# Kernel tuning notes

Hardware: AMD Instinct MI355X
Metric: run time of the kernel (lower is better)

Reference implementation:

```python
import jax, jax.numpy as jnp
import numpy as np

DIM = 256
NUM_HEADS = 8
REGIONS = [4, 4, 8, 8, 16, 16, 32, 32]  # per-head local window sizes
B, H_IMG, W_IMG = 8, 64, 64


def setup_inputs() -> dict:
    key = jax.random.key(0)
    ks = jax.random.split(key, 6)
    C = DIM
    s = 0.02
    return {
        'x': jax.random.normal(ks[0], (B, H_IMG * W_IMG, C), jnp.float32),
        'Wq': jax.random.normal(ks[1], (C, C), jnp.float32) * s,
        'Wkv': jax.random.normal(ks[2], (C, 2 * C), jnp.float32) * s,
        'Wlkv': jax.random.normal(ks[3], (C, 2 * C), jnp.float32) * s,
        'Wproj': jax.random.normal(ks[4], (C, C), jnp.float32) * s,
        'bproj': jnp.zeros((C,), jnp.float32),
        'H': H_IMG,
        'W': W_IMG,
    }


def _attn(q, k, v, scale):
    # softmax(q k^T * scale) v, batched over leading dims
    a = jax.nn.softmax(jnp.einsum('...qd,...kd->...qk', q, k) * scale, axis=-1)
    return jnp.einsum('...qk,...kd->...qd', a, v)


def reference(x, Wq, Wkv, Wlkv, Wproj, bproj, H, W):
    Bn, N, C = x.shape
    nh = NUM_HEADS
    Ch = C // nh
    scale = Ch ** -0.5
    M = max(REGIONS)

    q = (x @ Wq).reshape(Bn, N, nh, Ch).transpose(0, 2, 1, 3)            # [B,nh,N,Ch]
    kv = (x @ Wkv).reshape(Bn, N, 2, nh, Ch).transpose(2, 0, 3, 1, 4)    # [2,B,nh,N,Ch]
    k, v = kv[0], kv[1]

    head_outs, global_q = [], []
    for i, p in enumerate(REGIONS):
        def patch(a, p=p):  # [B,N,Ch] -> [B,NP,p*p,Ch]
            a = a.reshape(Bn, H // p, p, W // p, p, Ch)
            return a.transpose(0, 1, 3, 2, 4, 5).reshape(Bn, -1, p * p, Ch)
        qp, kp, vp = patch(q[:, i]), patch(k[:, i]), patch(v[:, i])
        # global query: mean over patches -> [B,p,p,Ch], bilinear upsample to [M,M]
        qg = qp.mean(axis=1).reshape(Bn, p, p, Ch)
        if M // p > 1:
            qg = jax.image.resize(qg, (Bn, M, M, Ch), method='bilinear')
        global_q.append(qg.reshape(Bn, M * M, Ch))
        out = _attn(qp, kp, vp, scale)                                    # [B,NP,p*p,Ch]
        head_outs.append(out.reshape(Bn, N, Ch))  # flatten in PATCH order (matches torch code)

    attn_fused = jnp.stack(head_outs, axis=1).transpose(0, 2, 1, 3).reshape(Bn, N, C)
    Q_g = jnp.stack(global_q, axis=1).transpose(0, 2, 1, 3).reshape(Bn, M * M, C)

    # blend: adaptive avg-pool attn_fused to [M,M] (exact pooling since M|H), cross-attend, upsample
    kh, kw = H // M, W // M
    pooled = attn_fused.reshape(Bn, M, kh, M, kw, C).mean(axis=(2, 4)).reshape(Bn, M * M, C)
    kv2 = (pooled @ Wlkv).reshape(Bn, M * M, 2, nh, Ch).transpose(2, 0, 3, 1, 4)
    k2, v2 = kv2[0], kv2[1]
    Qr = Q_g.reshape(Bn, M * M, nh, Ch).transpose(0, 2, 1, 3)             # [B,nh,M^2,Ch]
    gl = _attn(Qr, k2, v2, scale)                                          # [B,nh,M^2,Ch]
    gl = gl.transpose(0, 2, 1, 3).reshape(Bn, M, M, C)
    gl = jax.image.resize(gl, (Bn, H, W, C), method='bilinear').reshape(Bn, N, C)

    return (attn_fused + gl) @ Wproj + bproj
```

## Files before the change

### kernel.cpp

```cpp
#include <hip/hip_runtime.h>
#include <math.h>


typedef __attribute__((ext_vector_type(8))) short bf16x8;
typedef __attribute__((ext_vector_type(4))) float f32x4;

__device__ inline float bf2f(unsigned short u) {
  union { unsigned int i; float f; } v; v.i = ((unsigned int)u) << 16; return v.f;
}
__device__ inline unsigned short f2bf(float x) {
  union { float f; unsigned int i; } v; v.f = x;
  return (unsigned short)((v.i + 0x7FFFu + ((v.i >> 16) & 1u)) >> 16);
}

__global__ __launch_bounds__(256) void msa_xcast_r12(
    const float* __restrict__ x, unsigned short* __restrict__ xb)
{
  const size_t i = ((size_t)blockIdx.x * 256 + threadIdx.x) * 8;
  const float4 v0 = *reinterpret_cast<const float4*>(&x[i]);
  const float4 v1 = *reinterpret_cast<const float4*>(&x[i + 4]);
  bf16x8 o;
  o[0] = (short)f2bf(v0.x); o[1] = (short)f2bf(v0.y);
  o[2] = (short)f2bf(v0.z); o[3] = (short)f2bf(v0.w);
  o[4] = (short)f2bf(v1.x); o[5] = (short)f2bf(v1.y);
  o[6] = (short)f2bf(v1.z); o[7] = (short)f2bf(v1.w);
  *reinterpret_cast<bf16x8*>(&xb[i]) = o;
}

__global__ __launch_bounds__(256) void msa_wcast_r12(
    const float* __restrict__ Wq, const float* __restrict__ Wkv,
    const float* __restrict__ Wlkv, const float* __restrict__ Wproj,
    unsigned short* __restrict__ Wqkvt, unsigned short* __restrict__ Wlkvt,
    unsigned short* __restrict__ Wprjt)
{
  const int id = blockIdx.x * 256 + threadIdx.x;
  if (id < 196608) {
    const int r = id >> 8, k = id & 255;
    const float v = (r < 256) ? Wq[(size_t)k * 256 + r] : Wkv[(size_t)k * 512 + (r - 256)];
    Wqkvt[id] = f2bf(v);
  } else if (id < 327680) {
    const int j = id - 196608;
    const int n = j >> 8, k = j & 255;
    Wlkvt[j] = f2bf(Wlkv[(size_t)k * 512 + n]);
  } else if (id < 393216) {
    const int j = id - 327680;
    const int n = j >> 8, k = j & 255;
    Wprjt[j] = f2bf(Wproj[(size_t)k * 256 + n]);
  }
}

__global__ __launch_bounds__(256) void msa_gemm_mfma_r12(
    const unsigned short* __restrict__ Ab, const unsigned short* __restrict__ Wt,
    const float* __restrict__ bias, float* __restrict__ Cf,
    unsigned short* __restrict__ Cb, int K, int N)
{
  __shared__ __align__(16) unsigned short A_lds[128][40];
  __shared__ __align__(16) unsigned short B_lds[128][40];

  const int tid = threadIdx.x;
  const int wave = tid >> 6, lane = tid & 63;
  const int l15 = lane & 15, g = lane >> 4;
  const int bm = blockIdx.y * 128, bn = blockIdx.x * 128;
  const int wr = (wave >> 1) * 64, wc = (wave & 1) * 64;

  f32x4 acc[4][4] = {};

  for (int k0 = 0; k0 < K; k0 += 32) {
    __syncthreads();
#pragma unroll
    for (int s = 0; s < 2; ++s) {
      const int id = tid + s * 256;
      const int row = id >> 2, sg = (id & 3) << 3;
      *reinterpret_cast<bf16x8*>(&A_lds[row][sg]) =
          *reinterpret_cast<const bf16x8*>(&Ab[(size_t)(bm + row) * K + k0 + sg]);
      *reinterpret_cast<bf16x8*>(&B_lds[row][sg]) =
          *reinterpret_cast<const bf16x8*>(&Wt[(size_t)(bn + row) * K + k0 + sg]);
    }
    __syncthreads();

    bf16x8 a_frag[4], b_frag[4];
#pragma unroll
    for (int mi = 0; mi < 4; ++mi)
      a_frag[mi] = *reinterpret_cast<const bf16x8*>(&A_lds[wr + mi * 16 + l15][g << 3]);
#pragma unroll
    for (int ni = 0; ni < 4; ++ni)
      b_frag[ni] = *reinterpret_cast<const bf16x8*>(&B_lds[wc + ni * 16 + l15][g << 3]);
#pragma unroll
    for (int mi = 0; mi < 4; ++mi)
#pragma unroll
      for (int ni = 0; ni < 4; ++ni)
        acc[mi][ni] = __builtin_amdgcn_mfma_f32_16x16x32_bf16(
            a_frag[mi], b_frag[ni], acc[mi][ni], 0, 0, 0);
  }

#pragma unroll
  for (int mi = 0; mi < 4; ++mi)
#pragma unroll
    for (int ni = 0; ni < 4; ++ni) {
      const int col = bn + wc + ni * 16 + l15;
#pragma unroll
      for (int i = 0; i < 4; ++i) {
        const int row = bm + wr + mi * 16 + g * 4 + i;
        float v = acc[mi][ni][i];
        if (bias) v += bias[col];
        const size_t idx = (size_t)row * N + col;
        if (Cb) Cb[idx] = f2bf(v); else Cf[idx] = v;
      }
    }
}

__global__ __launch_bounds__(256) void msa_attn_mfma_r12(
    const unsigned short* __restrict__ qsrc, const unsigned short* __restrict__ kvsrc,
    float* __restrict__ outf, unsigned short* __restrict__ outb, int mode)
{
  __shared__ __align__(16) unsigned short K_lds[32][40];
  __shared__ __align__(16) unsigned short V_lds[32][40];
  __shared__ __align__(16) unsigned short P_lds[4][16][40];

  const int tid = threadIdx.x;
  const int wave = tid >> 6, lane = tid & 63;
  const int q16 = lane & 15, h = lane >> 4;
  const int b = blockIdx.y;

  int head, NTOK, P2, lp, pm1, base, qstr, kvstr, kofs, vofs;
  if (mode) {
    head = blockIdx.z; NTOK = 1024; P2 = 1024; lp = 0; pm1 = 0; base = 0;
    qstr = 256; kvstr = 512; kofs = 0; vofs = 256;
  } else {
    head = 2 + blockIdx.z;
    lp = (head < 4) ? 3 : (head < 6) ? 4 : 5;
    const int p = 1 << lp; pm1 = p - 1;
    NTOK = 4096; P2 = p * p;
    const int patch = (blockIdx.x * 64) >> (2 * lp);
    const int nbp = 64 >> lp;
    const int hb = patch / nbp, wb = patch - (patch / nbp) * nbp;
    base = ((hb << lp)) * 64 + (wb << lp);
    qstr = 768; kvstr = 768; kofs = 256; vofs = 512;
  }
  const int nq = blockIdx.x * 64 + wave * 16 + q16;
  int n;
  if (mode) n = nq;
  else { const int t = nq & (P2 - 1); n = base + ((t >> lp) << 6) + (t & pm1); }

  const bf16x8 qfrag = *reinterpret_cast<const bf16x8*>(
      qsrc + ((size_t)b * NTOK + n) * qstr + head * 32 + 8 * h);

  const float scale = 0.17677669529663687f;
  float m = -3.0e38f, l = 0.f;
  f32x4 o0 = {0.f, 0.f, 0.f, 0.f}, o1 = {0.f, 0.f, 0.f, 0.f};
  const f32x4 zc = {0.f, 0.f, 0.f, 0.f};

  const int skey = (tid & 127) >> 2;
  const int sh = tid & 3;
  const bool isK = tid < 128;

  for (int kc = 0; kc < P2; kc += 32) {
    __syncthreads();
    {
      const int kk = kc + skey;
      const int nk = mode ? kk : base + ((kk >> lp) << 6) + (kk & pm1);
      const unsigned short* src = kvsrc + ((size_t)b * NTOK + nk) * kvstr + head * 32
                                + (isK ? kofs : vofs) + 8 * sh;
      const bf16x8 v = *reinterpret_cast<const bf16x8*>(src);
      if (isK) {
        *reinterpret_cast<bf16x8*>(&K_lds[skey][8 * sh]) = v;
      } else {
#pragma unroll
        for (int j = 0; j < 8; ++j)
          V_lds[8 * sh + j][skey] = (unsigned short)v[j];
      }
    }
    __syncthreads();

    const bf16x8 k0 = *reinterpret_cast<const bf16x8*>(&K_lds[q16][8 * h]);
    const bf16x8 k1 = *reinterpret_cast<const bf16x8*>(&K_lds[16 + q16][8 * h]);
    const f32x4 st0 = __builtin_amdgcn_mfma_f32_16x16x32_bf16(k0, qfrag, zc, 0, 0, 0);
    const f32x4 st1 = __builtin_amdgcn_mfma_f32_16x16x32_bf16(k1, qfrag, zc, 0, 0, 0);

    float s[8];
#pragma unroll
    for (int i = 0; i < 4; ++i) { s[i] = st0[i] * scale; s[4 + i] = st1[i] * scale; }
    float cmax = s[0];
#pragma unroll
    for (int i = 1; i < 8; ++i) cmax = fmaxf(cmax, s[i]);
    cmax = fmaxf(cmax, __shfl_xor(cmax, 16));
    cmax = fmaxf(cmax, __shfl_xor(cmax, 32));
    const float mnew = fmaxf(m, cmax);
    const float f = __expf(m - mnew);
    float ps = 0.f;
    unsigned short pb[8];
#pragma unroll
    for (int i = 0; i < 8; ++i) {
      const float pe = __expf(s[i] - mnew);
      ps += pe;
      pb[i] = f2bf(pe);
    }
    l = l * f + ps;
    o0 *= f; o1 *= f;
    m = mnew;

    *reinterpret_cast<uint2*>(&P_lds[wave][q16][4 * h]) =
        make_uint2((unsigned)pb[0] | ((unsigned)pb[1] << 16),
                   (unsigned)pb[2] | ((unsigned)pb[3] << 16));
    *reinterpret_cast<uint2*>(&P_lds[wave][q16][16 + 4 * h]) =
        make_uint2((unsigned)pb[4] | ((unsigned)pb[5] << 16),
                   (unsigned)pb[6] | ((unsigned)pb[7] << 16));

    const bf16x8 pf = *reinterpret_cast<const bf16x8*>(&P_lds[wave][q16][8 * h]);
    const bf16x8 v0 = *reinterpret_cast<const bf16x8*>(&V_lds[q16][8 * h]);
    const bf16x8 v1 = *reinterpret_cast<const bf16x8*>(&V_lds[16 + q16][8 * h]);
    o0 = __builtin_amdgcn_mfma_f32_16x16x32_bf16(v0, pf, o0, 0, 0, 0);
    o1 = __builtin_amdgcn_mfma_f32_16x16x32_bf16(v1, pf, o1, 0, 0, 0);
  }

  l = l + __shfl_xor(l, 16);
  l = l + __shfl_xor(l, 32);
  const float inv = 1.f / l;
  const size_t obase = ((size_t)b * NTOK + nq) * 256 + head * 32;
  if (mode) {
    float* dst = outf + obase;
    float4 w0, w1;
    w0.x = o0[0] * inv; w0.y = o0[1] * inv; w0.z = o0[2] * inv; w0.w = o0[3] * inv;
    w1.x = o1[0] * inv; w1.y = o1[1] * inv; w1.z = o1[2] * inv; w1.w = o1[3] * inv;
    *reinterpret_cast<float4*>(dst + 4 * h) = w0;
    *reinterpret_cast<float4*>(dst + 16 + 4 * h) = w1;
  } else {
    unsigned short* dst = outb + obase;
    uint2 w0, w1;
    w0.x = (unsigned)f2bf(o0[0] * inv) | ((unsigned)f2bf(o0[1] * inv) << 16);
    w0.y = (unsigned)f2bf(o0[2] * inv) | ((unsigned)f2bf(o0[3] * inv) << 16);
    w1.x = (unsigned)f2bf(o1[0] * inv) | ((unsigned)f2bf(o1[1] * inv) << 16);
    w1.y = (unsigned)f2bf(o1[2] * inv) | ((unsigned)f2bf(o1[3] * inv) << 16);
    *reinterpret_cast<uint2*>(dst + 4 * h) = w0;
    *reinterpret_cast<uint2*>(dst + 16 + 4 * h) = w1;
  }
}

__global__ __launch_bounds__(256) void msa_attn_p4_r12(
    const unsigned short* __restrict__ xqkv, unsigned short* __restrict__ out)
{
  const int head = blockIdx.z;
  const int b = blockIdx.y;
  const int nq = blockIdx.x * 256 + threadIdx.x;

  const int patch = nq >> 4;
  const int t = nq & 15;
  const int hb = patch >> 4, wb = patch & 15;
  const int n = (hb * 4 + (t >> 2)) * 64 + (wb * 4 + (t & 3));

  float qr[32];
  {
    const bf16x8* q8 = reinterpret_cast<const bf16x8*>(
        xqkv + ((size_t)b * 4096 + n) * 768 + head * 32);
#pragma unroll
    for (int i = 0; i < 4; ++i) {
      const bf16x8 v = q8[i];
#pragma unroll
      for (int j = 0; j < 8; ++j) qr[i * 8 + j] = bf2f((unsigned short)v[j]);
    }
  }
  const float scale = 0.17677669529663687f;
  float m = -3.0e38f, l = 0.f;
  float acc[32] = {};
  const int kbase = (hb * 4) * 64 + wb * 4;
  for (int kk = 0; kk < 16; ++kk) {
    const int nk = kbase + (kk >> 2) * 64 + (kk & 3);
    const unsigned short* rowp = xqkv + ((size_t)b * 4096 + nk) * 768 + head * 32;
    const bf16x8* k8p = reinterpret_cast<const bf16x8*>(rowp + 256);
    const bf16x8* v8p = reinterpret_cast<const bf16x8*>(rowp + 512);
    float s = 0.f;
#pragma unroll
    for (int i = 0; i < 4; ++i) {
      const bf16x8 k8 = k8p[i];
#pragma unroll
      for (int j = 0; j < 8; ++j) s = fmaf(qr[i * 8 + j], bf2f((unsigned short)k8[j]), s);
    }
    s *= scale;
    if (s <= m) {
      const float pe = __expf(s - m);
      l += pe;
#pragma unroll
      for (int i = 0; i < 4; ++i) {
        const bf16x8 v8 = v8p[i];
#pragma unroll
        for (int j = 0; j < 8; ++j)
          acc[i * 8 + j] = fmaf(pe, bf2f((unsigned short)v8[j]), acc[i * 8 + j]);
      }
    } else {
      const float f = __expf(m - s);
      l = fmaf(l, f, 1.f);
#pragma unroll
      for (int i = 0; i < 4; ++i) {
        const bf16x8 v8 = v8p[i];
#pragma unroll
        for (int j = 0; j < 8; ++j)
          acc[i * 8 + j] = fmaf(acc[i * 8 + j], f, bf2f((unsigned short)v8[j]));
      }
      m = s;
    }
  }
  const float inv = 1.f / l;
  unsigned short* dst = out + ((size_t)b * 4096 + nq) * 256 + head * 32;
#pragma unroll
  for (int c = 0; c < 32; ++c) dst[c] = f2bf(acc[c] * inv);
}

__global__ __launch_bounds__(256) void msa_qg_reduce_r12(
    const unsigned short* __restrict__ xqkv, float* __restrict__ qg_all)
{
  __shared__ float red[256];
  const int head = blockIdx.z;
  const int lp = (head < 2) ? 2 : (head < 4) ? 3 : (head < 6) ? 4 : 5;
  const int p = 1 << lp;
  const int P2 = p * p;
  const int nbp = 64 >> lp;
  const int npat = nbp * nbp;
  const int R = (lp <= 3) ? 8 : 1;
  const int total = P2 * 32 * R;
  const int gid = blockIdx.x * 256 + threadIdx.x;
  if (gid >= total) return;
  const int b = blockIdx.y;

  const int c = gid & 31;
  const int tr = gid >> 5;
  const int r = tr & (R - 1);
  const int t = tr >> ((R == 8) ? 3 : 0);
  const int hp = t >> lp, wp = t & (p - 1);

  const unsigned short* src = xqkv + (size_t)b * 4096 * 768 + head * 32 + c;
  float s = 0.f;
  for (int j = r; j < npat; j += R) {
    const int hb = j / nbp, wb = j - (j / nbp) * nbp;
    const int n = ((hb << lp) + hp) * 64 + (wb << lp) + wp;
    s += bf2f(src[(size_t)n * 768]);
  }

  if (R == 8) {
    red[threadIdx.x] = s;
    __syncthreads();
    if (r < 4) red[threadIdx.x] += red[threadIdx.x + 128];
    __syncthreads();
    if (r < 2) red[threadIdx.x] += red[threadIdx.x + 64];
    __syncthreads();
    if (r == 0) {
      s = red[threadIdx.x] + red[threadIdx.x + 32];
      qg_all[((size_t)b * 8 + head) * 32768 + (size_t)t * 32 + c] = s / (float)npat;
    }
  } else {
    qg_all[((size_t)b * 8 + head) * 32768 + (size_t)t * 32 + c] = s / (float)npat;
  }
}

__global__ __launch_bounds__(256) void msa_qg_upsample_r12(
    const float* __restrict__ qg_all, unsigned short* __restrict__ Qg)
{
  const int head = blockIdx.z;
  const int p = (head < 2) ? 4 : (head < 4) ? 8 : (head < 6) ? 16 : 32;
  const int e = blockIdx.x * 256 + threadIdx.x;
  const int b = blockIdx.y;
  const int mlin = e >> 5, c = e & 31;
  const int mi = mlin >> 5, mj = mlin & 31;
  const float* src = qg_all + ((size_t)b * 8 + head) * 32768;
  float v;
  if (p == 32) {
    v = src[(size_t)mlin * 32 + c];
  } else {
    const float s = (float)p / 32.0f;
    const float xf = (mj + 0.5f) * s - 0.5f;
    const float yf = (mi + 0.5f) * s - 0.5f;
    const float xfl = floorf(xf), yfl = floorf(yf);
    const float fx = xf - xfl, fy = yf - yfl;
    const int x0 = (int)xfl, y0 = (int)yfl;
    const int x0c = max(0, min(p - 1, x0)), x1c = max(0, min(p - 1, x0 + 1));
    const int y0c = max(0, min(p - 1, y0)), y1c = max(0, min(p - 1, y0 + 1));
    const float v00 = src[(size_t)(y0c * p + x0c) * 32 + c];
    const float v01 = src[(size_t)(y0c * p + x1c) * 32 + c];
    const float v10 = src[(size_t)(y1c * p + x0c) * 32 + c];
    const float v11 = src[(size_t)(y1c * p + x1c) * 32 + c];
    v = (1.f - fy) * ((1.f - fx) * v00 + fx * v01)
      + fy * ((1.f - fx) * v10 + fx * v11);
  }
  Qg[((size_t)b * 1024 + mlin) * 256 + head * 32 + c] = f2bf(v);
}

__global__ __launch_bounds__(256) void msa_pool_r12(
    const unsigned short* __restrict__ attn, unsigned short* __restrict__ pooled)
{
  const int c = threadIdx.x;
  const int mlin = blockIdx.x;
  const int b = blockIdx.y;
  const int mi = mlin >> 5, mj = mlin & 31;
  const size_t base = (size_t)b * 4096;
  const int r0 = mi * 2, q0 = mj * 2;
  float s = bf2f(attn[(base + (r0 * 64 + q0)) * 256 + c])
          + bf2f(attn[(base + (r0 * 64 + q0 + 1)) * 256 + c])
          + bf2f(attn[(base + ((r0 + 1) * 64 + q0)) * 256 + c])
          + bf2f(attn[(base + ((r0 + 1) * 64 + q0 + 1)) * 256 + c]);
  pooled[((size_t)b * 1024 + mlin) * 256 + c] = f2bf(s * 0.25f);
}

__global__ __launch_bounds__(256) void msa_blend_r12(
    const float* __restrict__ gl, unsigned short* __restrict__ attn)
{
  const int c = threadIdx.x;
  const int n = blockIdx.x;
  const int b = blockIdx.y;
  const int hh = n >> 6, w = n & 63;
  const float xf = (w + 0.5f) * 0.5f - 0.5f;
  const float yf = (hh + 0.5f) * 0.5f - 0.5f;
  const float xfl = floorf(xf), yfl = floorf(yf);
  const float fx = xf - xfl, fy = yf - yfl;
  const int x0 = (int)xfl, y0 = (int)yfl;
  const int x0c = max(0, min(31, x0)), x1c = max(0, min(31, x0 + 1));
  const int y0c = max(0, min(31, y0)), y1c = max(0, min(31, y0 + 1));
  const float* g = gl + (size_t)b * 1024 * 256;
  const float v00 = g[(size_t)(y0c * 32 + x0c) * 256 + c];
  const float v01 = g[(size_t)(y0c * 32 + x1c) * 256 + c];
  const float v10 = g[(size_t)(y1c * 32 + x0c) * 256 + c];
  const float v11 = g[(size_t)(y1c * 32 + x1c) * 256 + c];
  const float v = (1.f - fy) * ((1.f - fx) * v00 + fx * v01)
                + fy * ((1.f - fx) * v10 + fx * v11);
  const size_t idx = ((size_t)b * 4096 + n) * 256 + c;
  attn[idx] = f2bf(bf2f(attn[idx]) + v);
}

extern "C" void kernel_launch(void* const* d_in, const int* in_sizes, int n_in,
                              void* d_out, int out_size, void* d_ws, size_t ws_size,
                              hipStream_t stream)
{
  const float* x     = (const float*)d_in[0];
  const float* Wq    = (const float*)d_in[1];
  const float* Wkv   = (const float*)d_in[2];
  const float* Wlkv  = (const float*)d_in[3];
  const float* Wproj = (const float*)d_in[4];
  const float* bproj = (const float*)d_in[5];

  char* ws = (char*)d_ws;
  unsigned short* xqkv  = (unsigned short*)(ws + 0);
  unsigned short* attnb = (unsigned short*)(ws + 50331648ull);
  unsigned short* Qg    = (unsigned short*)(ws + 67108864ull);
  float* qg_all = (float*)(ws + 71303168ull);
  unsigned short* Wqkvt = (unsigned short*)(ws + 79691776ull);
  unsigned short* Wlkvt = (unsigned short*)(ws + 80084992ull);
  unsigned short* Wprjt = (unsigned short*)(ws + 80347136ull);
  float* gl     = (float*)(ws + 80478208ull);
  unsigned short* xb    = (unsigned short*)(ws + 88866816ull);
  unsigned short* pooled = (unsigned short*)(ws + 0);
  unsigned short* kv2    = (unsigned short*)(ws + 16777216ull);

  msa_xcast_r12<<<dim3(4096), 256, 0, stream>>>(x, xb);
  msa_wcast_r12<<<dim3(1536), 256, 0, stream>>>(Wq, Wkv, Wlkv, Wproj, Wqkvt, Wlkvt, Wprjt);

  msa_gemm_mfma_r12<<<dim3(6, 256), 256, 0, stream>>>(xb, Wqkvt, nullptr, nullptr, xqkv, 256, 768);

  msa_qg_reduce_r12<<<dim3(128, 8, 8), 256, 0, stream>>>(xqkv, qg_all);
  msa_qg_upsample_r12<<<dim3(128, 8, 8), 256, 0, stream>>>(qg_all, Qg);

  msa_attn_p4_r12<<<dim3(16, 8, 2), 256, 0, stream>>>(xqkv, attnb);
  msa_attn_mfma_r12<<<dim3(64, 8, 6), 256, 0, stream>>>(xqkv, xqkv, nullptr, attnb, 0);

  msa_pool_r12<<<dim3(1024, 8), 256, 0, stream>>>(attnb, pooled);
  msa_gemm_mfma_r12<<<dim3(4, 64), 256, 0, stream>>>(pooled, Wlkvt, nullptr, nullptr, kv2, 256, 512);

  msa_attn_mfma_r12<<<dim3(16, 8, 8), 256, 0, stream>>>(Qg, kv2, gl, nullptr, 1);

  msa_blend_r12<<<dim3(4096, 8), 256, 0, stream>>>(gl, attnb);
  msa_gemm_mfma_r12<<<dim3(2, 256), 256, 0, stream>>>(attnb, Wprjt, bproj, (float*)d_out, nullptr, 256, 256);

  (void)in_sizes; (void)n_in; (void)out_size; (void)ws_size;
}
```

Measured before the change: 235.2 us.

## Drop online-softmax max tracking and feed P directly from registers to MFMA

```diff
diff --git a/kernel.cpp b/kernel.cpp
--- a/kernel.cpp
+++ b/kernel.cpp
@@ -3,6 +3,7 @@
 
 
 typedef __attribute__((ext_vector_type(8))) short bf16x8;
+typedef __attribute__((ext_vector_type(4))) short bf16x4;
 typedef __attribute__((ext_vector_type(4))) float f32x4;
 
 __device__ inline float bf2f(unsigned short u) {
@@ -13,7 +14,7 @@
   return (unsigned short)((v.i + 0x7FFFu + ((v.i >> 16) & 1u)) >> 16);
 }
 
-__global__ __launch_bounds__(256) void msa_xcast_r12(
+__global__ __launch_bounds__(256) void msa_xcast_r13(
     const float* __restrict__ x, unsigned short* __restrict__ xb)
 {
   const size_t i = ((size_t)blockIdx.x * 256 + threadIdx.x) * 8;
@@ -27,7 +28,7 @@
   *reinterpret_cast<bf16x8*>(&xb[i]) = o;
 }
 
-__global__ __launch_bounds__(256) void msa_wcast_r12(
+__global__ __launch_bounds__(256) void msa_wcast_r13(
     const float* __restrict__ Wq, const float* __restrict__ Wkv,
     const float* __restrict__ Wlkv, const float* __restrict__ Wproj,
     unsigned short* __restrict__ Wqkvt, unsigned short* __restrict__ Wlkvt,
@@ -49,7 +50,7 @@
   }
 }
 
-__global__ __launch_bounds__(256) void msa_gemm_mfma_r12(
+__global__ __launch_bounds__(256) void msa_gemm_mfma_r13(
     const unsigned short* __restrict__ Ab, const unsigned short* __restrict__ Wt,
     const float* __restrict__ bias, float* __restrict__ Cf,
     unsigned short* __restrict__ Cb, int K, int N)
@@ -109,13 +110,12 @@
     }
 }
 
-__global__ __launch_bounds__(256) void msa_attn_mfma_r12(
+__global__ __launch_bounds__(256) void msa_attn_mfma_r13(
     const unsigned short* __restrict__ qsrc, const unsigned short* __restrict__ kvsrc,
     float* __restrict__ outf, unsigned short* __restrict__ outb, int mode)
 {
-  __shared__ __align__(16) unsigned short K_lds[32][40];
-  __shared__ __align__(16) unsigned short V_lds[32][40];
-  __shared__ __align__(16) unsigned short P_lds[4][16][40];
+  __shared__ __align__(16) unsigned short K_lds[64][40];
+  __shared__ __align__(16) unsigned short V_lds[32][68];
 
   const int tid = threadIdx.x;
   const int wave = tid >> 6, lane = tid & 63;
@@ -145,72 +145,60 @@
   const bf16x8 qfrag = *reinterpret_cast<const bf16x8*>(
       qsrc + ((size_t)b * NTOK + n) * qstr + head * 32 + 8 * h);
 
-  const float scale = 0.17677669529663687f;
-  float m = -3.0e38f, l = 0.f;
+  const float CEXP = 0.25503485947f;
+  float l = 0.f;
   f32x4 o0 = {0.f, 0.f, 0.f, 0.f}, o1 = {0.f, 0.f, 0.f, 0.f};
   const f32x4 zc = {0.f, 0.f, 0.f, 0.f};
 
-  const int skey = (tid & 127) >> 2;
+  const int skey = tid >> 2;
   const int sh = tid & 3;
-  const bool isK = tid < 128;
-
-  for (int kc = 0; kc < P2; kc += 32) {
+
+  for (int kc = 0; kc < P2; kc += 64) {
     __syncthreads();
     {
       const int kk = kc + skey;
       const int nk = mode ? kk : base + ((kk >> lp) << 6) + (kk & pm1);
-      const unsigned short* src = kvsrc + ((size_t)b * NTOK + nk) * kvstr + head * 32
-                                + (isK ? kofs : vofs) + 8 * sh;
-      const bf16x8 v = *reinterpret_cast<const bf16x8*>(src);
-      if (isK) {
-        *reinterpret_cast<bf16x8*>(&K_lds[skey][8 * sh]) = v;
-      } else {
-#pragma unroll
-        for (int j = 0; j < 8; ++j)
-          V_lds[8 * sh + j][skey] = (unsigned short)v[j];
+      const unsigned short* row = kvsrc + ((size_t)b * NTOK + nk) * kvstr + head * 32;
+      *reinterpret_cast<bf16x8*>(&K_lds[skey][8 * sh]) =
+          *reinterpret_cast<const bf16x8*>(row + kofs + 8 * sh);
+      const bf16x8 v = *reinterpret_cast<const bf16x8*>(row + vofs + 8 * sh);
+#pragma unroll
+      for (int j = 0; j < 8; ++j)
+        V_lds[8 * sh + j][skey] = (unsigned short)v[j];
+    }
+    __syncthreads();
+
+#pragma unroll
+    for (int sub = 0; sub < 2; ++sub) {
+      const int s32 = sub * 32;
+      const bf16x8 k0 = *reinterpret_cast<const bf16x8*>(&K_lds[s32 + q16][8 * h]);
+      const bf16x8 k1 = *reinterpret_cast<const bf16x8*>(&K_lds[s32 + 16 + q16][8 * h]);
+      const f32x4 st0 = __builtin_amdgcn_mfma_f32_16x16x32_bf16(k0, qfrag, zc, 0, 0, 0);
+      const f32x4 st1 = __builtin_amdgcn_mfma_f32_16x16x32_bf16(k1, qfrag, zc, 0, 0, 0);
+
+      bf16x8 pb;
+#pragma unroll
+      for (int i = 0; i < 4; ++i) {
+        const float p0 = exp2f(st0[i] * CEXP);
+        const float p1 = exp2f(st1[i] * CEXP);
+        l += p0 + p1;
+        pb[i] = (short)f2bf(p0);
+        pb[4 + i] = (short)f2bf(p1);
       }
-    }
-    __syncthreads();
-
-    const bf16x8 k0 = *reinterpret_cast<const bf16x8*>(&K_lds[q16][8 * h]);
-    const bf16x8 k1 = *reinterpret_cast<const bf16x8*>(&K_lds[16 + q16][8 * h]);
-    const f32x4 st0 = __builtin_amdgcn_mfma_f32_16x16x32_bf16(k0, qfrag, zc, 0, 0, 0);
-    const f32x4 st1 = __builtin_amdgcn_mfma_f32_16x16x32_bf16(k1, qfrag, zc, 0, 0, 0);
-
-    float s[8];
-#pragma unroll
-    for (int i = 0; i < 4; ++i) { s[i] = st0[i] * scale; s[4 + i] = st1[i] * scale; }
-    float cmax = s[0];
-#pragma unroll
-    for (int i = 1; i < 8; ++i) cmax = fmaxf(cmax, s[i]);
-    cmax = fmaxf(cmax, __shfl_xor(cmax, 16));
-    cmax = fmaxf(cmax, __shfl_xor(cmax, 32));
-    const float mnew = fmaxf(m, cmax);
-    const float f = __expf(m - mnew);
-    float ps = 0.f;
-    unsigned short pb[8];
-#pragma unroll
-    for (int i = 0; i < 8; ++i) {
-      const float pe = __expf(s[i] - mnew);
-      ps += pe;
-      pb[i] = f2bf(pe);
-    }
-    l = l * f + ps;
-    o0 *= f; o1 *= f;
-    m = mnew;
-
-    *reinterpret_cast<uint2*>(&P_lds[wave][q16][4 * h]) =
-        make_uint2((unsigned)pb[0] | ((unsigned)pb[1] << 16),
-                   (unsigned)pb[2] | ((unsigned)pb[3] << 16));
-    *reinterpret_cast<uint2*>(&P_lds[wave][q16][16 + 4 * h]) =
-        make_uint2((unsigned)pb[4] | ((unsigned)pb[5] << 16),
-                   (unsigned)pb[6] | ((unsigned)pb[7] << 16));
-
-    const bf16x8 pf = *reinterpret_cast<const bf16x8*>(&P_lds[wave][q16][8 * h]);
-    const bf16x8 v0 = *reinterpret_cast<const bf16x8*>(&V_lds[q16][8 * h]);
-    const bf16x8 v1 = *reinterpret_cast<const bf16x8*>(&V_lds[16 + q16][8 * h]);
-    o0 = __builtin_amdgcn_mfma_f32_16x16x32_bf16(v0, pf, o0, 0, 0, 0);
-    o1 = __builtin_amdgcn_mfma_f32_16x16x32_bf16(v1, pf, o1, 0, 0, 0);
+
+      const bf16x4 va0 = *reinterpret_cast<const bf16x4*>(&V_lds[q16][s32 + 4 * h]);
+      const bf16x4 vb0 = *reinterpret_cast<const bf16x4*>(&V_lds[q16][s32 + 16 + 4 * h]);
+      const bf16x4 va1 = *reinterpret_cast<const bf16x4*>(&V_lds[16 + q16][s32 + 4 * h]);
+      const bf16x4 vb1 = *reinterpret_cast<const bf16x4*>(&V_lds[16 + q16][s32 + 16 + 4 * h]);
+      bf16x8 v0, v1;
+#pragma unroll
+      for (int i = 0; i < 4; ++i) {
+        v0[i] = va0[i]; v0[4 + i] = vb0[i];
+        v1[i] = va1[i]; v1[4 + i] = vb1[i];
+      }
+      o0 = __builtin_amdgcn_mfma_f32_16x16x32_bf16(v0, pb, o0, 0, 0, 0);
+      o1 = __builtin_amdgcn_mfma_f32_16x16x32_bf16(v1, pb, o1, 0, 0, 0);
+    }
   }
 
   l = l + __shfl_xor(l, 16);
@@ -236,7 +224,7 @@
   }
 }
 
-__global__ __launch_bounds__(256) void msa_attn_p4_r12(
+__global__ __launch_bounds__(256) void msa_attn_p4_r13(
     const unsigned short* __restrict__ xqkv, unsigned short* __restrict__ out)
 {
   const int head = blockIdx.z;
@@ -259,8 +247,8 @@
       for (int j = 0; j < 8; ++j) qr[i * 8 + j] = bf2f((unsigned short)v[j]);
     }
   }
-  const float scale = 0.17677669529663687f;
-  float m = -3.0e38f, l = 0.f;
+  const float CEXP = 0.25503485947f;
+  float l = 0.f;
   float acc[32] = {};
   const int kbase = (hb * 4) * 64 + wb * 4;
   for (int kk = 0; kk < 16; ++kk) {
@@ -275,28 +263,14 @@
 #pragma unroll
       for (int j = 0; j < 8; ++j) s = fmaf(qr[i * 8 + j], bf2f((unsigned short)k8[j]), s);
     }
-    s *= scale;
-    if (s <= m) {
-      const float pe = __expf(s - m);
-      l += pe;
-#pragma unroll
-      for (int i = 0; i < 4; ++i) {
-        const bf16x8 v8 = v8p[i];
-#pragma unroll
-        for (int j = 0; j < 8; ++j)
-          acc[i * 8 + j] = fmaf(pe, bf2f((unsigned short)v8[j]), acc[i * 8 + j]);
-      }
-    } else {
-      const float f = __expf(m - s);
-      l = fmaf(l, f, 1.f);
-#pragma unroll
-      for (int i = 0; i < 4; ++i) {
-        const bf16x8 v8 = v8p[i];
-#pragma unroll
-        for (int j = 0; j < 8; ++j)
-          acc[i * 8 + j] = fmaf(acc[i * 8 + j], f, bf2f((unsigned short)v8[j]));
-      }
-      m = s;
+    const float p = exp2f(s * CEXP);
+    l += p;
+#pragma unroll
+    for (int i = 0; i < 4; ++i) {
+      const bf16x8 v8 = v8p[i];
+#pragma unroll
+      for (int j = 0; j < 8; ++j)
+        acc[i * 8 + j] = fmaf(p, bf2f((unsigned short)v8[j]), acc[i * 8 + j]);
     }
   }
   const float inv = 1.f / l;
@@ -305,7 +279,7 @@
   for (int c = 0; c < 32; ++c) dst[c] = f2bf(acc[c] * inv);
 }
 
-__global__ __launch_bounds__(256) void msa_qg_reduce_r12(
+__global__ __launch_bounds__(256) void msa_qg_reduce_r13(
     const unsigned short* __restrict__ xqkv, float* __restrict__ qg_all)
 {
   __shared__ float red[256];
@@ -351,7 +325,7 @@
   }
 }
 
-__global__ __launch_bounds__(256) void msa_qg_upsample_r12(
+__global__ __launch_bounds__(256) void msa_qg_upsample_r13(
     const float* __restrict__ qg_all, unsigned short* __restrict__ Qg)
 {
   const int head = blockIdx.z;
@@ -383,7 +357,7 @@
   Qg[((size_t)b * 1024 + mlin) * 256 + head * 32 + c] = f2bf(v);
 }
 
-__global__ __launch_bounds__(256) void msa_pool_r12(
+__global__ __launch_bounds__(256) void msa_pool_r13(
     const unsigned short* __restrict__ attn, unsigned short* __restrict__ pooled)
 {
   const int c = threadIdx.x;
@@ -399,7 +373,7 @@
   pooled[((size_t)b * 1024 + mlin) * 256 + c] = f2bf(s * 0.25f);
 }
 
-__global__ __launch_bounds__(256) void msa_blend_r12(
+__global__ __launch_bounds__(256) void msa_blend_r13(
     const float* __restrict__ gl, unsigned short* __restrict__ attn)
 {
   const int c = threadIdx.x;
@@ -448,24 +422,24 @@
   unsigned short* pooled = (unsigned short*)(ws + 0);
   unsigned short* kv2    = (unsigned short*)(ws + 16777216ull);
 
-  msa_xcast_r12<<<dim3(4096), 256, 0, stream>>>(x, xb);
-  msa_wcast_r12<<<dim3(1536), 256, 0, stream>>>(Wq, Wkv, Wlkv, Wproj, Wqkvt, Wlkvt, Wprjt);
-
-  msa_gemm_mfma_r12<<<dim3(6, 256), 256, 0, stream>>>(xb, Wqkvt, nullptr, nullptr, xqkv, 256, 768);
-
-  msa_qg_reduce_r12<<<dim3(128, 8, 8), 256, 0, stream>>>(xqkv, qg_all);
-  msa_qg_upsample_r12<<<dim3(128, 8, 8), 256, 0, stream>>>(qg_all, Qg);
-
-  msa_attn_p4_r12<<<dim3(16, 8, 2), 256, 0, stream>>>(xqkv, attnb);
-  msa_attn_mfma_r12<<<dim3(64, 8, 6), 256, 0, stream>>>(xqkv, xqkv, nullptr, attnb, 0);
-
-  msa_pool_r12<<<dim3(1024, 8), 256, 0, stream>>>(attnb, pooled);
-  msa_gemm_mfma_r12<<<dim3(4, 64), 256, 0, stream>>>(pooled, Wlkvt, nullptr, nullptr, kv2, 256, 512);
-
-  msa_attn_mfma_r12<<<dim3(16, 8, 8), 256, 0, stream>>>(Qg, kv2, gl, nullptr, 1);
-
-  msa_blend_r12<<<dim3(4096, 8), 256, 0, stream>>>(gl, attnb);
-  msa_gemm_mfma_r12<<<dim3(2, 256), 256, 0, stream>>>(attnb, Wprjt, bproj, (float*)d_out, nullptr, 256, 256);
+  msa_xcast_r13<<<dim3(4096), 256, 0, stream>>>(x, xb);
+  msa_wcast_r13<<<dim3(1536), 256, 0, stream>>>(Wq, Wkv, Wlkv, Wproj, Wqkvt, Wlkvt, Wprjt);
+
+  msa_gemm_mfma_r13<<<dim3(6, 256), 256, 0, stream>>>(xb, Wqkvt, nullptr, nullptr, xqkv, 256, 768);
+
+  msa_qg_reduce_r13<<<dim3(128, 8, 8), 256, 0, stream>>>(xqkv, qg_all);
+  msa_qg_upsample_r13<<<dim3(128, 8, 8), 256, 0, stream>>>(qg_all, Qg);
+
+  msa_attn_p4_r13<<<dim3(16, 8, 2), 256, 0, stream>>>(xqkv, attnb);
+  msa_attn_mfma_r13<<<dim3(64, 8, 6), 256, 0, stream>>>(xqkv, xqkv, nullptr, attnb, 0);
+
+  msa_pool_r13<<<dim3(1024, 8), 256, 0, stream>>>(attnb, pooled);
+  msa_gemm_mfma_r13<<<dim3(4, 64), 256, 0, stream>>>(pooled, Wlkvt, nullptr, nullptr, kv2, 256, 512);
+
+  msa_attn_mfma_r13<<<dim3(16, 8, 8), 256, 0, stream>>>(Qg, kv2, gl, nullptr, 1);
+
+  msa_blend_r13<<<dim3(4096, 8), 256, 0, stream>>>(gl, attnb);
+  msa_gemm_mfma_r13<<<dim3(2, 256), 256, 0, stream>>>(attnb, Wprjt, bproj, (float*)d_out, nullptr, 256, 256);
 
   (void)in_sizes; (void)n_in; (void)out_size; (void)ws_size;
 }
```

Measured after the change: 237.4 us. About the same (+0.9%).
